# Optimization experiments

Measured on AMD Instinct MI355X. Metric: run time of the kernel, lower is better.

The kernel has to match this reference:

```python
import jax, jax.numpy as jnp
import numpy as np
from jax import lax

B, H, T, K = 32, 384, 1024, 3
MAX_LEN = 4096  # fixed ragged-output capacity (pad/mask for jit)
EPS = 1e-5


def conv1d_same(x, W, b):
    # x: [B,H,T], W: [H_out,H_in,K] -> [B,H,T] with SAME padding
    y = lax.conv_general_dilated(x, W, (1,), 'SAME',
                                 dimension_numbers=('NCH', 'OIH', 'NCH'))
    return y + b[None, :, None]


def layernorm_ch(x, g, b):
    # LayerNorm over the channel (hidden) dim of [B,H,T]
    m = jnp.mean(x, axis=1, keepdims=True)
    v = jnp.var(x, axis=1, keepdims=True)
    return (x - m) * lax.rsqrt(v + EPS) * g[None, :, None] + b[None, :, None]


def setup_inputs() -> dict:
    key = jax.random.key(0)
    ks = jax.random.split(key, 4)
    s = 0.02  # small init so floor(exp(relu(z))) gives modest durations
    x = jax.random.normal(ks[0], (B, H, T), dtype=jnp.float32)
    W1 = jax.random.normal(ks[1], (H, H, K), dtype=jnp.float32) * s
    W2 = jax.random.normal(ks[2], (H, H, K), dtype=jnp.float32) * s
    Wl = jax.random.normal(ks[3], (H, 1), dtype=jnp.float32) * s
    z = jnp.zeros((H,), jnp.float32)
    o = jnp.ones((H,), jnp.float32)
    return {'x': x, 'W1': W1, 'b1': z, 'g1': o, 'be1': z,
            'W2': W2, 'b2': z, 'g2': o, 'be2': z,
            'Wl': Wl, 'bl': jnp.zeros((1,), jnp.float32)}


def reference(x, W1, b1, g1, be1, W2, b2, g2, be2, Wl, bl):
    h = jax.nn.relu(layernorm_ch(conv1d_same(x, W1, b1), g1, be1))
    h = jax.nn.relu(layernorm_ch(conv1d_same(h, W2, b2), g2, be2))
    # Linear(H,1) applied per timestep, then ReLU
    z = jax.nn.relu(jnp.einsum('bht,h->bt', h, Wl[:, 0]) + bl[0])  # [B,T]
    durations = jnp.floor(jnp.exp(z)).astype(jnp.int32)            # [B,T]
    # ragged repeat_interleave along time, padded to MAX_LEN:
    cum = jnp.cumsum(durations, axis=-1)                           # [B,T]
    pos = jnp.arange(MAX_LEN)
    idx = jax.vmap(lambda c: jnp.searchsorted(c, pos, side='right'))(cum)  # [B,MAX]
    valid = (pos[None, :] < cum[:, -1:]).astype(x.dtype)           # [B,MAX]
    idx_c = jnp.minimum(idx, T - 1)
    aligned = jnp.take_along_axis(x, idx_c[:, None, :], axis=-1) * valid[:, None, :]
    return durations, aligned
```

## Files before the change

### kernel.cpp

```cpp
#include <hip/hip_runtime.h>
#include <hip/hip_bf16.h>


#define BB 32
#define HHD 384
#define TTOT 1024
#define MAXL 4096

typedef _Float16 half8 __attribute__((ext_vector_type(8)));
typedef float floatx4 __attribute__((ext_vector_type(4)));

__global__ void prep_w_kernel(const float* __restrict__ W1,
                              const float* __restrict__ W2,
                              _Float16* __restrict__ q1h, _Float16* __restrict__ q1l,
                              _Float16* __restrict__ q2h, _Float16* __restrict__ q2l) {
    const int e = blockIdx.x * 256 + threadIdx.x;
    const float* W = blockIdx.y ? W2 : W1;
    _Float16* oh = blockIdx.y ? q2h : q1h;
    _Float16* ol = blockIdx.y ? q2l : q1l;
    const int d  = e & 31;
    const int m  = (e >> 5) % 384;
    const int ck = e / (32 * 384);
    const int c  = ck / 3, k = ck - 3 * c;
    const float w = W[(size_t)m * 1152 + (size_t)(32 * c + d) * 3 + k];
    const _Float16 hi = (_Float16)w;
    oh[e] = hi;
    ol[e] = (_Float16)((w - (float)hi) * 2048.0f);
}

__global__ void prep_x_kernel(const float* __restrict__ X,
                              _Float16* __restrict__ o1,
                              _Float16* __restrict__ o2) {
    __shared__ float Ls[64][65];
    const int h0 = blockIdx.x * 64;
    const int t0 = blockIdx.y * 64;
    const int b  = blockIdx.z;
    const int tid = threadIdx.x;
    const int tl = tid & 63, hq = tid >> 6;
    const float* Xb = X + (size_t)b * HHD * TTOT;
#pragma unroll
    for (int i = 0; i < 16; ++i) {
        const int h = i * 4 + hq;
        Ls[tl][h] = Xb[(size_t)(h0 + h) * TTOT + t0 + tl];
    }
    __syncthreads();
#pragma unroll
    for (int i = 0; i < 16; ++i) {
        const int t = i * 4 + hq;
        const float v = Ls[t][tl];
        const _Float16 a = (_Float16)v;
        const size_t o = ((size_t)b * TTOT + t0 + t) * HHD + h0 + tl;
        o1[o] = a;
        o2[o] = (_Float16)((v - (float)a) * 2048.0f);
    }
}

__launch_bounds__(256, 2)
__global__ void conv_mfma_kernel(const _Float16* __restrict__ Bh,
                                 const _Float16* __restrict__ Bl,
                                 const _Float16* __restrict__ Ah,
                                 const _Float16* __restrict__ Al,
                                 const float* __restrict__ bias,
                                 float* __restrict__ Out) {
    __shared__ __align__(16) _Float16 sm[33440];
    const int tid  = threadIdx.x;
    const int lane = tid & 63, wid = tid >> 6;
    const int wm = wid >> 1, wn = wid & 1;
    const int l15 = lane & 15, g4 = lane >> 4;
    const int h0 = blockIdx.x * 96;
    const int t0 = blockIdx.y * 128;
    const int b  = blockIdx.z;

    floatx4 ahh[3][4], axx[3][4];
#pragma unroll
    for (int mt = 0; mt < 3; ++mt)
#pragma unroll
        for (int nt = 0; nt < 4; ++nt) {
            ahh[mt][nt] = (floatx4){0.f, 0.f, 0.f, 0.f};
            axx[mt][nt] = (floatx4){0.f, 0.f, 0.f, 0.f};
        }

    const size_t xbase = (size_t)b * TTOT * HHD;

    for (int ch = 0; ch < 12; ++ch) {
        __syncthreads();
#pragma unroll
        for (int it = 0; it < 9; ++it) {
            const int e  = tid + it * 256;
            const int s  = e / 1152;
            const int r1 = e - s * 1152;
            const int k  = r1 / 384;
            const int q  = r1 - k * 384;
            const int m  = q >> 2, c8 = (q & 3) << 3;
            const _Float16* src = (s ? Al : Ah) +
                ((size_t)((ch * 3 + k) * 384 + h0 + m) << 5) + c8;
            const uint4 v = *(const uint4*)src;
            *(uint4*)&sm[((s * 3 + k) * 96 + m) * 40 + c8] = v;
        }
#pragma unroll
        for (int it = 0; it < 5; ++it) {
            const int e = tid + it * 256;
            if (e < 1040) {
                const int s  = e / 520;
                const int r1 = e - s * 520;
                const int j  = r1 >> 2, q = r1 & 3;
                const int gt = t0 - 1 + j;
                uint4 v = make_uint4(0u, 0u, 0u, 0u);
                if (gt >= 0 && gt < TTOT) {
                    const _Float16* src = (s ? Bl : Bh) + xbase +
                        (size_t)gt * HHD + ch * 32 + (q << 3);
                    v = *(const uint4*)src;
                }
                *(uint4*)&sm[23040 + (s * 130 + j) * 40 + (q << 3)] = v;
            }
        }
        __syncthreads();

#pragma unroll
        for (int k = 0; k < 3; ++k) {
            half8 ah[3], al[3], bh[4], bl[4];
#pragma unroll
            for (int mt = 0; mt < 3; ++mt) {
                const int m = wm * 48 + mt * 16 + l15;
                ah[mt] = *(const half8*)&sm[((0 + k) * 96 + m) * 40 + g4 * 8];
                al[mt] = *(const half8*)&sm[((3 + k) * 96 + m) * 40 + g4 * 8];
            }
#pragma unroll
            for (int nt = 0; nt < 4; ++nt) {
                const int j = wn * 64 + nt * 16 + l15 + k;
                bh[nt] = *(const half8*)&sm[23040 + (0   + j) * 40 + g4 * 8];
                bl[nt] = *(const half8*)&sm[23040 + (130 + j) * 40 + g4 * 8];
            }
#pragma unroll
            for (int mt = 0; mt < 3; ++mt)
#pragma unroll
                for (int nt = 0; nt < 4; ++nt) {
                    ahh[mt][nt] = __builtin_amdgcn_mfma_f32_16x16x32_f16(
                        ah[mt], bh[nt], ahh[mt][nt], 0, 0, 0);
                    axx[mt][nt] = __builtin_amdgcn_mfma_f32_16x16x32_f16(
                        ah[mt], bl[nt], axx[mt][nt], 0, 0, 0);
                    axx[mt][nt] = __builtin_amdgcn_mfma_f32_16x16x32_f16(
                        al[mt], bh[nt], axx[mt][nt], 0, 0, 0);
                }
        }
    }

    __syncthreads();
    float* Lt = (float*)sm;
#pragma unroll
    for (int mt = 0; mt < 3; ++mt)
#pragma unroll
        for (int nt = 0; nt < 4; ++nt) {
            const int row = wn * 64 + nt * 16 + l15;
            const int col = wm * 48 + mt * 16 + g4 * 4;
            float4 v;
            v.x = ahh[mt][nt][0] + axx[mt][nt][0] * (1.0f / 2048.0f);
            v.y = ahh[mt][nt][1] + axx[mt][nt][1] * (1.0f / 2048.0f);
            v.z = ahh[mt][nt][2] + axx[mt][nt][2] * (1.0f / 2048.0f);
            v.w = ahh[mt][nt][3] + axx[mt][nt][3] * (1.0f / 2048.0f);
            *(float4*)&Lt[row * 100 + col] = v;
        }
    __syncthreads();
    const size_t obase = ((size_t)b * TTOT + t0) * HHD + h0;
#pragma unroll
    for (int i = 0; i < 12; ++i) {
        const int e = tid + i * 256;
        const int row = e / 24, c4 = (e - row * 24) * 4;
        float4 v = *(const float4*)&Lt[row * 100 + c4];
        const float4 bv = *(const float4*)&bias[h0 + c4];
        v.x += bv.x; v.y += bv.y; v.z += bv.z; v.w += bv.w;
        *(float4*)&Out[obase + (size_t)row * HHD + c4] = v;
    }
}

__global__ void ln_split_kernel(const float* __restrict__ hraw,
                                const float* __restrict__ g,
                                const float* __restrict__ be,
                                _Float16* __restrict__ o1,
                                _Float16* __restrict__ o2) {
    const int row = blockIdx.x * 4 + (threadIdx.x >> 6);
    const int ln  = threadIdx.x & 63;
    const float* src = hraw + (size_t)row * HHD;
    float v[6], s = 0.f, ss = 0.f;
#pragma unroll
    for (int j = 0; j < 6; ++j) { v[j] = src[ln + 64 * j]; s += v[j]; ss += v[j] * v[j]; }
#pragma unroll
    for (int m = 32; m >= 1; m >>= 1) { s += __shfl_xor(s, m, 64); ss += __shfl_xor(ss, m, 64); }
    const float mean = s * (1.f / HHD);
    const float var  = ss * (1.f / HHD) - mean * mean;
    const float inv  = rsqrtf(var + 1e-5f);
#pragma unroll
    for (int j = 0; j < 6; ++j) {
        const int h = ln + 64 * j;
        float y = (v[j] - mean) * inv * g[h] + be[h];
        y = fmaxf(y, 0.f);
        const _Float16 a = (_Float16)y;
        const size_t o = (size_t)row * HHD + h;
        o1[o] = a;
        o2[o] = (_Float16)((y - (float)a) * 2048.0f);
    }
}

__global__ void ln_proj_kernel(const float* __restrict__ hraw,
                               const float* __restrict__ g,
                               const float* __restrict__ be,
                               const float* __restrict__ Wl,
                               const float* __restrict__ blp,
                               float* __restrict__ zb) {
    const int row = blockIdx.x * 4 + (threadIdx.x >> 6);
    const int ln  = threadIdx.x & 63;
    const float* src = hraw + (size_t)row * HHD;
    float v[6], s = 0.f, ss = 0.f;
#pragma unroll
    for (int j = 0; j < 6; ++j) { v[j] = src[ln + 64 * j]; s += v[j]; ss += v[j] * v[j]; }
#pragma unroll
    for (int m = 32; m >= 1; m >>= 1) { s += __shfl_xor(s, m, 64); ss += __shfl_xor(ss, m, 64); }
    const float mean = s * (1.f / HHD);
    const float inv  = rsqrtf(ss * (1.f / HHD) - mean * mean + 1e-5f);
    float zs = 0.f;
#pragma unroll
    for (int j = 0; j < 6; ++j) {
        const int h = ln + 64 * j;
        float y = (v[j] - mean) * inv * g[h] + be[h];
        zs += fmaxf(y, 0.f) * Wl[h];
    }
#pragma unroll
    for (int m = 32; m >= 1; m >>= 1) zs += __shfl_xor(zs, m, 64);
    if (ln == 0) zb[row] = fmaxf(zs + blp[0], 0.f);
}

__global__ void dur_scan_kernel(const float* __restrict__ z,
                                float* __restrict__ durOut,
                                int* __restrict__ cum) {
    __shared__ int sb[TTOT];
    const int b = blockIdx.x;
    const int t = threadIdx.x;
    const int d = (int)floorf(expf(z[b * TTOT + t]));
    durOut[b * TTOT + t] = (float)d;
    sb[t] = d;
    __syncthreads();
    for (int off = 1; off < TTOT; off <<= 1) {
        const int v = (t >= off) ? sb[t - off] : 0;
        __syncthreads();
        sb[t] += v;
        __syncthreads();
    }
    cum[b * TTOT + t] = sb[t];
}

__global__ void gather_kernel(const float* __restrict__ X,
                              const int* __restrict__ cum,
                              float* __restrict__ aligned) {
    __shared__ int cs[TTOT];
    const int b   = blockIdx.y;
    const int tid = threadIdx.x;
    for (int e = tid; e < TTOT; e += 256) cs[e] = cum[b * TTOT + e];
    __syncthreads();
    const int pos   = blockIdx.x * 256 + tid;
    const int total = cs[TTOT - 1];
    int lo = 0, hi = TTOT;
    while (lo < hi) {
        const int mid = (lo + hi) >> 1;
        if (cs[mid] <= pos) lo = mid + 1; else hi = mid;
    }
    const float vmul = (pos < total) ? 1.f : 0.f;
    const int idx = min(lo, TTOT - 1);
    const float* Xb = X + (size_t)b * HHD * TTOT;
    float* Ab = aligned + (size_t)b * HHD * MAXL;
#pragma unroll 4
    for (int h = 0; h < HHD; ++h)
        Ab[(size_t)h * MAXL + pos] = Xb[(size_t)h * TTOT + idx] * vmul;
}

extern "C" void kernel_launch(void* const* d_in, const int* in_sizes, int n_in,
                              void* d_out, int out_size, void* d_ws, size_t ws_size,
                              hipStream_t stream) {
    const float* x   = (const float*)d_in[0];
    const float* W1  = (const float*)d_in[1];
    const float* b1  = (const float*)d_in[2];
    const float* g1  = (const float*)d_in[3];
    const float* be1 = (const float*)d_in[4];
    const float* W2  = (const float*)d_in[5];
    const float* b2  = (const float*)d_in[6];
    const float* g2  = (const float*)d_in[7];
    const float* be2 = (const float*)d_in[8];
    const float* Wl  = (const float*)d_in[9];
    const float* bl  = (const float*)d_in[10];

    float* out     = (float*)d_out;
    float* durOut  = out;
    float* aligned = out + (size_t)BB * TTOT;
    float* h_raw   = aligned;

    char* ws = (char*)d_ws;
    const size_t wqB = (size_t)442368 * sizeof(_Float16);
    const size_t xtB = (size_t)BB * TTOT * HHD * sizeof(_Float16);
    _Float16* Wq1h = (_Float16*)(ws);
    _Float16* Wq1l = (_Float16*)(ws + wqB);
    _Float16* Wq2h = (_Float16*)(ws + 2 * wqB);
    _Float16* Wq2l = (_Float16*)(ws + 3 * wqB);
    _Float16* Xt1  = (_Float16*)(ws + 4 * wqB);
    _Float16* Xt2  = (_Float16*)(ws + 4 * wqB + xtB);
    float*    zb   = (float*)   (ws + 4 * wqB + 2 * xtB);
    int*      cum  = (int*)     (ws + 4 * wqB + 2 * xtB + (size_t)BB * TTOT * 4);

    prep_w_kernel<<<dim3(1728, 2), 256, 0, stream>>>(W1, W2, Wq1h, Wq1l, Wq2h, Wq2l);
    prep_x_kernel<<<dim3(6, 16, 32), 256, 0, stream>>>(x, Xt1, Xt2);
    conv_mfma_kernel<<<dim3(4, 8, 32), 256, 0, stream>>>(Xt1, Xt2, Wq1h, Wq1l, b1, h_raw);
    ln_split_kernel<<<8192, 256, 0, stream>>>(h_raw, g1, be1, Xt1, Xt2);
    conv_mfma_kernel<<<dim3(4, 8, 32), 256, 0, stream>>>(Xt1, Xt2, Wq2h, Wq2l, b2, h_raw);
    ln_proj_kernel<<<8192, 256, 0, stream>>>(h_raw, g2, be2, Wl, bl, zb);
    dur_scan_kernel<<<BB, TTOT, 0, stream>>>(zb, durOut, cum);
    gather_kernel<<<dim3(MAXL / 256, BB), 256, 0, stream>>>(x, cum, aligned);
}
```

Baseline: 515.8 us.

## Vectorize memory access in prep, layernorm, scan and gather kernels

Reworks several auxiliary kernels to use wide vector loads and stores. prep_x transposes through shared memory and writes half8 packs; both layernorm kernels read float4 pairs per lane with 48 active lanes; the duration scan moves from a 1024-thread shared-memory Hillis-Steele scan to a 256-thread wave shuffle scan; gather now writes float4 along the output position and splits the hidden dimension across more blocks. The aim is fewer memory transactions and less synchronization in the memory-bound stages, at the cost of idle lanes in the layernorm kernels and redundant cum loads per gather block.

```diff
diff --git a/kernel.cpp b/kernel.cpp
--- a/kernel.cpp
+++ b/kernel.cpp
@@ -36,22 +36,29 @@
     const int t0 = blockIdx.y * 64;
     const int b  = blockIdx.z;
     const int tid = threadIdx.x;
-    const int tl = tid & 63, hq = tid >> 6;
+    const int tl = tid & 63, w = tid >> 6;
     const float* Xb = X + (size_t)b * HHD * TTOT;
 #pragma unroll
     for (int i = 0; i < 16; ++i) {
-        const int h = i * 4 + hq;
-        Ls[tl][h] = Xb[(size_t)(h0 + h) * TTOT + t0 + tl];
-    }
-    __syncthreads();
-#pragma unroll
-    for (int i = 0; i < 16; ++i) {
-        const int t = i * 4 + hq;
-        const float v = Ls[t][tl];
-        const _Float16 a = (_Float16)v;
-        const size_t o = ((size_t)b * TTOT + t0 + t) * HHD + h0 + tl;
-        o1[o] = a;
-        o2[o] = (_Float16)((v - (float)a) * 2048.0f);
+        const int h = i * 4 + w;
+        Ls[h][tl] = Xb[(size_t)(h0 + h) * TTOT + t0 + tl];
+    }
+    __syncthreads();
+    const int g = tl >> 3, q = tl & 7;
+#pragma unroll
+    for (int j = 0; j < 2; ++j) {
+        const int tloc = w * 16 + j * 8 + g;
+        half8 vh, vl;
+#pragma unroll
+        for (int i = 0; i < 8; ++i) {
+            const float f = Ls[8 * q + i][tloc];
+            const _Float16 a = (_Float16)f;
+            vh[i] = a;
+            vl[i] = (_Float16)((f - (float)a) * 2048.0f);
+        }
+        const size_t o = ((size_t)b * TTOT + t0 + tloc) * HHD + h0 + 8 * q;
+        *(half8*)&o1[o] = vh;
+        *(half8*)&o2[o] = vl;
     }
 }
 
@@ -179,25 +186,48 @@
                                 _Float16* __restrict__ o1,
                                 _Float16* __restrict__ o2) {
     const int row = blockIdx.x * 4 + (threadIdx.x >> 6);
-    const int ln  = threadIdx.x & 63;
+    const int l   = threadIdx.x & 63;
     const float* src = hraw + (size_t)row * HHD;
-    float v[6], s = 0.f, ss = 0.f;
-#pragma unroll
-    for (int j = 0; j < 6; ++j) { v[j] = src[ln + 64 * j]; s += v[j]; ss += v[j] * v[j]; }
-#pragma unroll
-    for (int m = 32; m >= 1; m >>= 1) { s += __shfl_xor(s, m, 64); ss += __shfl_xor(ss, m, 64); }
+    float4 va = {0, 0, 0, 0}, vb = {0, 0, 0, 0};
+    if (l < 48) {
+        va = *(const float4*)&src[8 * l];
+        vb = *(const float4*)&src[8 * l + 4];
+    }
+    float s  = va.x + va.y + va.z + va.w + vb.x + vb.y + vb.z + vb.w;
+    float ss = va.x * va.x + va.y * va.y + va.z * va.z + va.w * va.w +
+               vb.x * vb.x + vb.y * vb.y + vb.z * vb.z + vb.w * vb.w;
+#pragma unroll
+    for (int m = 32; m >= 1; m >>= 1) {
+        s  += __shfl_xor(s, m, 64);
+        ss += __shfl_xor(ss, m, 64);
+    }
     const float mean = s * (1.f / HHD);
-    const float var  = ss * (1.f / HHD) - mean * mean;
-    const float inv  = rsqrtf(var + 1e-5f);
-#pragma unroll
-    for (int j = 0; j < 6; ++j) {
-        const int h = ln + 64 * j;
-        float y = (v[j] - mean) * inv * g[h] + be[h];
-        y = fmaxf(y, 0.f);
-        const _Float16 a = (_Float16)y;
-        const size_t o = (size_t)row * HHD + h;
-        o1[o] = a;
-        o2[o] = (_Float16)((y - (float)a) * 2048.0f);
+    const float inv  = rsqrtf(ss * (1.f / HHD) - mean * mean + 1e-5f);
+    if (l < 48) {
+        const float4 ga = *(const float4*)&g[8 * l];
+        const float4 gb = *(const float4*)&g[8 * l + 4];
+        const float4 ba = *(const float4*)&be[8 * l];
+        const float4 bb = *(const float4*)&be[8 * l + 4];
+        float y[8];
+        y[0] = (va.x - mean) * inv * ga.x + ba.x;
+        y[1] = (va.y - mean) * inv * ga.y + ba.y;
+        y[2] = (va.z - mean) * inv * ga.z + ba.z;
+        y[3] = (va.w - mean) * inv * ga.w + ba.w;
+        y[4] = (vb.x - mean) * inv * gb.x + bb.x;
+        y[5] = (vb.y - mean) * inv * gb.y + bb.y;
+        y[6] = (vb.z - mean) * inv * gb.z + bb.z;
+        y[7] = (vb.w - mean) * inv * gb.w + bb.w;
+        half8 vh, vl;
+#pragma unroll
+        for (int i = 0; i < 8; ++i) {
+            const float r = fmaxf(y[i], 0.f);
+            const _Float16 a = (_Float16)r;
+            vh[i] = a;
+            vl[i] = (_Float16)((r - (float)a) * 2048.0f);
+        }
+        const size_t o = (size_t)row * HHD + 8 * l;
+        *(half8*)&o1[o] = vh;
+        *(half8*)&o2[o] = vl;
     }
 }
 
@@ -208,68 +238,117 @@
                                const float* __restrict__ blp,
                                float* __restrict__ zb) {
     const int row = blockIdx.x * 4 + (threadIdx.x >> 6);
-    const int ln  = threadIdx.x & 63;
+    const int l   = threadIdx.x & 63;
     const float* src = hraw + (size_t)row * HHD;
-    float v[6], s = 0.f, ss = 0.f;
-#pragma unroll
-    for (int j = 0; j < 6; ++j) { v[j] = src[ln + 64 * j]; s += v[j]; ss += v[j] * v[j]; }
-#pragma unroll
-    for (int m = 32; m >= 1; m >>= 1) { s += __shfl_xor(s, m, 64); ss += __shfl_xor(ss, m, 64); }
+    float4 va = {0, 0, 0, 0}, vb = {0, 0, 0, 0};
+    if (l < 48) {
+        va = *(const float4*)&src[8 * l];
+        vb = *(const float4*)&src[8 * l + 4];
+    }
+    float s  = va.x + va.y + va.z + va.w + vb.x + vb.y + vb.z + vb.w;
+    float ss = va.x * va.x + va.y * va.y + va.z * va.z + va.w * va.w +
+               vb.x * vb.x + vb.y * vb.y + vb.z * vb.z + vb.w * vb.w;
+#pragma unroll
+    for (int m = 32; m >= 1; m >>= 1) {
+        s  += __shfl_xor(s, m, 64);
+        ss += __shfl_xor(ss, m, 64);
+    }
     const float mean = s * (1.f / HHD);
     const float inv  = rsqrtf(ss * (1.f / HHD) - mean * mean + 1e-5f);
     float zs = 0.f;
-#pragma unroll
-    for (int j = 0; j < 6; ++j) {
-        const int h = ln + 64 * j;
-        float y = (v[j] - mean) * inv * g[h] + be[h];
-        zs += fmaxf(y, 0.f) * Wl[h];
+    if (l < 48) {
+        const float4 ga = *(const float4*)&g[8 * l];
+        const float4 gb = *(const float4*)&g[8 * l + 4];
+        const float4 ba = *(const float4*)&be[8 * l];
+        const float4 bb = *(const float4*)&be[8 * l + 4];
+        const float4 wa = *(const float4*)&Wl[8 * l];
+        const float4 wb = *(const float4*)&Wl[8 * l + 4];
+        zs += fmaxf((va.x - mean) * inv * ga.x + ba.x, 0.f) * wa.x;
+        zs += fmaxf((va.y - mean) * inv * ga.y + ba.y, 0.f) * wa.y;
+        zs += fmaxf((va.z - mean) * inv * ga.z + ba.z, 0.f) * wa.z;
+        zs += fmaxf((va.w - mean) * inv * ga.w + ba.w, 0.f) * wa.w;
+        zs += fmaxf((vb.x - mean) * inv * gb.x + bb.x, 0.f) * wb.x;
+        zs += fmaxf((vb.y - mean) * inv * gb.y + bb.y, 0.f) * wb.y;
+        zs += fmaxf((vb.z - mean) * inv * gb.z + bb.z, 0.f) * wb.z;
+        zs += fmaxf((vb.w - mean) * inv * gb.w + bb.w, 0.f) * wb.w;
     }
 #pragma unroll
     for (int m = 32; m >= 1; m >>= 1) zs += __shfl_xor(zs, m, 64);
-    if (ln == 0) zb[row] = fmaxf(zs + blp[0], 0.f);
+    if (l == 0) zb[row] = fmaxf(zs + blp[0], 0.f);
 }
 
 __global__ void dur_scan_kernel(const float* __restrict__ z,
                                 float* __restrict__ durOut,
                                 int* __restrict__ cum) {
-    __shared__ int sb[TTOT];
+    __shared__ int wsum[4];
     const int b = blockIdx.x;
-    const int t = threadIdx.x;
-    const int d = (int)floorf(expf(z[b * TTOT + t]));
-    durOut[b * TTOT + t] = (float)d;
-    sb[t] = d;
-    __syncthreads();
-    for (int off = 1; off < TTOT; off <<= 1) {
-        const int v = (t >= off) ? sb[t - off] : 0;
-        __syncthreads();
-        sb[t] += v;
-        __syncthreads();
-    }
-    cum[b * TTOT + t] = sb[t];
+    const int tid = threadIdx.x;
+    const int l = tid & 63, w = tid >> 6;
+    const float4 zv = *(const float4*)&z[b * TTOT + tid * 4];
+    int d0 = (int)floorf(expf(zv.x));
+    int d1 = (int)floorf(expf(zv.y));
+    int d2 = (int)floorf(expf(zv.z));
+    int d3 = (int)floorf(expf(zv.w));
+    *(float4*)&durOut[b * TTOT + tid * 4] =
+        make_float4((float)d0, (float)d1, (float)d2, (float)d3);
+    const int s4 = d0 + d1 + d2 + d3;
+    int sc = s4;
+#pragma unroll
+    for (int off = 1; off <= 32; off <<= 1) {
+        const int v = __shfl_up(sc, off, 64);
+        if (l >= off) sc += v;
+    }
+    if (l == 63) wsum[w] = sc;
+    __syncthreads();
+    int base = 0;
+#pragma unroll
+    for (int j = 0; j < 4; ++j)
+        if (j < w) base += wsum[j];
+    const int ex = base + sc - s4;
+    int4 c;
+    c.x = ex + d0; c.y = c.x + d1; c.z = c.y + d2; c.w = c.z + d3;
+    *(int4*)&cum[b * TTOT + tid * 4] = c;
 }
 
 __global__ void gather_kernel(const float* __restrict__ X,
                               const int* __restrict__ cum,
                               float* __restrict__ aligned) {
     __shared__ int cs[TTOT];
-    const int b   = blockIdx.y;
+    const int pt = blockIdx.x, ht = blockIdx.y, b = blockIdx.z;
     const int tid = threadIdx.x;
-    for (int e = tid; e < TTOT; e += 256) cs[e] = cum[b * TTOT + e];
-    __syncthreads();
-    const int pos   = blockIdx.x * 256 + tid;
+#pragma unroll
+    for (int i = 0; i < 4; ++i) cs[tid + 256 * i] = cum[b * TTOT + tid + 256 * i];
+    __syncthreads();
+
     const int total = cs[TTOT - 1];
+    const int pos0 = pt * 1024 + tid * 4;
     int lo = 0, hi = TTOT;
     while (lo < hi) {
         const int mid = (lo + hi) >> 1;
-        if (cs[mid] <= pos) lo = mid + 1; else hi = mid;
-    }
-    const float vmul = (pos < total) ? 1.f : 0.f;
-    const int idx = min(lo, TTOT - 1);
+        if (cs[mid] <= pos0) lo = mid + 1; else hi = mid;
+    }
+    int id0 = lo;
+    int id1 = (id0 < TTOT && cs[id0] <= pos0 + 1) ? id0 + 1 : id0;
+    int id2 = (id1 < TTOT && cs[id1] <= pos0 + 2) ? id1 + 1 : id1;
+    int id3 = (id2 < TTOT && cs[id2] <= pos0 + 3) ? id2 + 1 : id2;
+    const float m0 = (pos0     < total) ? 1.f : 0.f;
+    const float m1 = (pos0 + 1 < total) ? 1.f : 0.f;
+    const float m2 = (pos0 + 2 < total) ? 1.f : 0.f;
+    const float m3 = (pos0 + 3 < total) ? 1.f : 0.f;
+    const int i0 = min(id0, TTOT - 1), i1 = min(id1, TTOT - 1);
+    const int i2 = min(id2, TTOT - 1), i3 = min(id3, TTOT - 1);
+
     const float* Xb = X + (size_t)b * HHD * TTOT;
     float* Ab = aligned + (size_t)b * HHD * MAXL;
-#pragma unroll 4
-    for (int h = 0; h < HHD; ++h)
-        Ab[(size_t)h * MAXL + pos] = Xb[(size_t)h * TTOT + idx] * vmul;
+#pragma unroll 8
+    for (int hh = 0; hh < 48; ++hh) {
+        const int h = ht * 48 + hh;
+        const float* xr = Xb + (size_t)h * TTOT;
+        float4 v;
+        v.x = xr[i0] * m0; v.y = xr[i1] * m1;
+        v.z = xr[i2] * m2; v.w = xr[i3] * m3;
+        *(float4*)&Ab[(size_t)h * MAXL + pos0] = v;
+    }
 }
 
 extern "C" void kernel_launch(void* const* d_in, const int* in_sizes, int n_in,
@@ -310,6 +389,6 @@
     ln_split_kernel<<<8192, 256, 0, stream>>>(h_raw, g1, be1, Xt1, Xt2);
     conv_mfma_kernel<<<dim3(4, 8, 32), 256, 0, stream>>>(Xt1, Xt2, Wq2h, Wq2l, b2, h_raw);
     ln_proj_kernel<<<8192, 256, 0, stream>>>(h_raw, g2, be2, Wl, bl, zb);
-    dur_scan_kernel<<<BB, TTOT, 0, stream>>>(zb, durOut, cum);
-    gather_kernel<<<dim3(MAXL / 256, BB), 256, 0, stream>>>(x, cum, aligned);
-}
+    dur_scan_kernel<<<BB, 256, 0, stream>>>(zb, durOut, cum);
+    gather_kernel<<<dim3(4, 8, BB), 256, 0, stream>>>(x, cum, aligned);
+}
```

New measurement: 565.0 us. +9.6%, slower.
